# Optimization experiments

Measured on AMD Instinct MI355X. Metric: run time of the kernel, lower is better.

The kernel has to match this reference:

```python
import jax, jax.numpy as jnp
import numpy as np

B, S, D_IN, RANK, D_OUT = 8, 1024, 1280, 64, 1280
DOWN_SIZE = RANK * D_IN      # 81920
UP_SIZE = D_OUT * RANK       # 81920


def setup_inputs() -> dict:
    key = jax.random.key(0)
    k1, k2 = jax.random.split(key)
    x = jax.random.normal(k1, (B, S, D_IN), dtype=jnp.float32)
    # per-image embedding that encodes the dynamic LoRA weights
    embed = jax.random.normal(k2, (B, DOWN_SIZE + UP_SIZE), dtype=jnp.float32) * 0.02
    return {"x": x, "embed": embed}


def reference(x, embed):
    # down_forward: per-sample weight = embed[:, :down_size].view(down_shape)=[rank, d_in]
    # original does x_chunk @ W.T per sample; batched as a single grouped GEMM
    w_down = embed[:, :DOWN_SIZE].reshape(B, RANK, D_IN)   # [B, r, d_in]
    h = jnp.einsum('bsd,brd->bsr', x, w_down)              # x @ W_down.T, batched
    # up_forward: per-sample weight = embed[:, -up_size:].view(up_shape)=[d_out, rank]
    w_up = embed[:, -UP_SIZE:].reshape(B, D_OUT, RANK)     # [B, d_out, r]
    out = jnp.einsum('bsr,bor->bso', h, w_up)              # h @ W_up.T, batched
    return out
```

## Files before the change

### kernel.cpp

```cpp
#include <hip/hip_runtime.h>

#define NB   8
#define S_   1024
#define DIN  1280
#define RANK 64
#define DOUT 1280
#define DOWN (RANK * DIN)
#define EMB  (DOWN + DOUT * RANK)
#define XSTRIDE 1288

typedef __bf16 bf16x8 __attribute__((ext_vector_type(8)));
typedef __bf16 bf16x4 __attribute__((ext_vector_type(4)));
typedef float  f32x4  __attribute__((ext_vector_type(4)));

__device__ __forceinline__ bf16x8 cvt8(float4 f0, float4 f1) {
    bf16x8 v;
    v[0]=(__bf16)f0.x; v[1]=(__bf16)f0.y; v[2]=(__bf16)f0.z; v[3]=(__bf16)f0.w;
    v[4]=(__bf16)f1.x; v[5]=(__bf16)f1.y; v[6]=(__bf16)f1.z; v[7]=(__bf16)f1.w;
    return v;
}

__global__ __launch_bounds__(512, 2) void lora_fused(const float* __restrict__ x,
                                                     const float* __restrict__ embed,
                                                     float* __restrict__ out) {
    __shared__ __bf16 xls[16 * XSTRIDE];
    __shared__ float  pbuf[4][16][20];
    __shared__ __bf16 hld[16][80];

    const int b    = blockIdx.x & 7;
    const int s0   = (blockIdx.x >> 3) * 16;
    const int t    = threadIdx.x;
    const int w    = t >> 6;
    const int l    = t & 63;
    const int quad = l >> 4;
    const int lc   = l & 15;
    const int dq   = quad * 8;

    {
        const int row = t >> 5;
        const int c   = t & 31;
        const float4* src = reinterpret_cast<const float4*>(x + (size_t)(b * S_ + s0 + row) * DIN);
        __bf16* drow = xls + row * XSTRIDE;
#pragma unroll
        for (int j = 0; j < 10; ++j) {
            float4 f = src[c + 32 * j];
            bf16x4 v;
            v[0]=(__bf16)f.x; v[1]=(__bf16)f.y; v[2]=(__bf16)f.z; v[3]=(__bf16)f.w;
            *reinterpret_cast<bf16x4*>(drow + c * 4 + 128 * j) = v;
        }
    }
    __syncthreads();

    const int nt = w & 3;
    const int kh = w >> 2;
    const float*  wdrow  = embed + (size_t)b * EMB + (size_t)(nt * 16 + lc) * DIN + kh * 640;
    const __bf16* xlsrow = xls + lc * XSTRIDE + kh * 640;

    f32x4 acc = {0,0,0,0};
#pragma unroll 5
    for (int ks = 0; ks < 20; ++ks) {
        const int k = ks * 32 + dq;
        bf16x8 af = *reinterpret_cast<const bf16x8*>(xlsrow + k);
        const float4* wp = reinterpret_cast<const float4*>(wdrow + k);
        bf16x8 bf = cvt8(wp[0], wp[1]);
        acc = __builtin_amdgcn_mfma_f32_16x16x32_bf16(af, bf, acc, 0, 0, 0);
    }

    if (kh == 1) {
#pragma unroll
        for (int i = 0; i < 4; ++i) pbuf[nt][quad * 4 + i][lc] = acc[i];
    }
    __syncthreads();
    if (kh == 0) {
#pragma unroll
        for (int i = 0; i < 4; ++i) {
            float v = acc[i] + pbuf[nt][quad * 4 + i][lc];
            hld[quad * 4 + i][nt * 16 + lc] = (__bf16)v;
        }
    }
    __syncthreads();

    bf16x8 ha0 = *reinterpret_cast<const bf16x8*>(&hld[lc][dq]);
    bf16x8 ha1 = *reinterpret_cast<const bf16x8*>(&hld[lc][32 + dq]);
    const float* wu    = embed + (size_t)b * EMB + DOWN;
    float*       obase = out + (size_t)(b * S_ + s0 + quad * 4) * DOUT;

#pragma unroll 2
    for (int tt = 0; tt < 10; ++tt) {
        const int n = w + 8 * tt;
        const int o = n * 16 + lc;
        const float4* wr = reinterpret_cast<const float4*>(wu + (size_t)o * RANK);
        const int q2 = quad * 2;
        bf16x8 b0 = cvt8(wr[q2],     wr[q2 + 1]);
        bf16x8 b1 = cvt8(wr[8 + q2], wr[9 + q2]);
        f32x4 c = {0,0,0,0};
        c = __builtin_amdgcn_mfma_f32_16x16x32_bf16(ha0, b0, c, 0, 0, 0);
        c = __builtin_amdgcn_mfma_f32_16x16x32_bf16(ha1, b1, c, 0, 0, 0);
#pragma unroll
        for (int i = 0; i < 4; ++i)
            obase[(size_t)i * DOUT + o] = c[i];
    }
}

extern "C" void kernel_launch(void* const* d_in, const int* in_sizes, int n_in,
                              void* d_out, int out_size, void* d_ws, size_t ws_size,
                              hipStream_t stream) {
    const float* x     = (const float*)d_in[0];
    const float* embed = (const float*)d_in[1];
    float*       out   = (float*)d_out;
    (void)in_sizes; (void)n_in; (void)out_size; (void)d_ws; (void)ws_size;

    lora_fused<<<dim3(512), dim3(512), 0, stream>>>(x, embed, out);
}
```

Baseline: 124.5 us.

## Software-pipeline embed weight loads with register double buffering in both GEMM stages

The down-projection weight loads from embed are now issued before the x staging and shared-memory barrier, and prefetched one group ahead into double-buffered registers. The up-projection weights for the next output tile are prefetched while the current MFMAs and stores run. The aim is to hide global-load latency behind the x conversion, the barriers and the MFMA work. In exchange, register use rises considerably (roughly 20 float4 buffers plus 10 for x), which may cut occupancy under launch_bounds(512,2) or cause spills.

```diff
diff --git a/kernel.cpp b/kernel.cpp
--- a/kernel.cpp
+++ b/kernel.cpp
@@ -35,70 +35,96 @@
     const int quad = l >> 4;
     const int lc   = l & 15;
     const int dq   = quad * 8;
+    const int q2   = quad * 2;
+
+    const int nt = w & 3;
+    const int kh = w >> 2;
+    const float4* wq =
+        reinterpret_cast<const float4*>(embed + (size_t)b * EMB + (size_t)(nt * 16 + lc) * DIN + kh * 640);
 
     {
         const int row = t >> 5;
         const int c   = t & 31;
         const float4* src = reinterpret_cast<const float4*>(x + (size_t)(b * S_ + s0 + row) * DIN);
+        float4 f[10];
+#pragma unroll
+        for (int j = 0; j < 10; ++j) f[j] = src[c + 32 * j];
+
+        float4 wA[10], wB[10];
+#pragma unroll
+        for (int j = 0; j < 5; ++j) { wA[2*j] = wq[j*8 + q2]; wA[2*j+1] = wq[j*8 + q2 + 1]; }
+
         __bf16* drow = xls + row * XSTRIDE;
 #pragma unroll
         for (int j = 0; j < 10; ++j) {
-            float4 f = src[c + 32 * j];
             bf16x4 v;
-            v[0]=(__bf16)f.x; v[1]=(__bf16)f.y; v[2]=(__bf16)f.z; v[3]=(__bf16)f.w;
+            v[0]=(__bf16)f[j].x; v[1]=(__bf16)f[j].y; v[2]=(__bf16)f[j].z; v[3]=(__bf16)f[j].w;
             *reinterpret_cast<bf16x4*>(drow + c * 4 + 128 * j) = v;
         }
-    }
-    __syncthreads();
+        __syncthreads();
 
-    const int nt = w & 3;
-    const int kh = w >> 2;
-    const float*  wdrow  = embed + (size_t)b * EMB + (size_t)(nt * 16 + lc) * DIN + kh * 640;
-    const __bf16* xlsrow = xls + lc * XSTRIDE + kh * 640;
+        const __bf16* xlsrow = xls + lc * XSTRIDE + kh * 640;
+        f32x4 acc = {0,0,0,0};
+#pragma unroll
+        for (int g = 0; g < 4; ++g) {
+            float4* cur = (g & 1) ? wB : wA;
+            float4* nxt = (g & 1) ? wA : wB;
+            if (g < 3) {
+#pragma unroll
+                for (int j = 0; j < 5; ++j) {
+                    nxt[2*j]   = wq[(g+1)*40 + j*8 + q2];
+                    nxt[2*j+1] = wq[(g+1)*40 + j*8 + q2 + 1];
+                }
+            }
+#pragma unroll
+            for (int j = 0; j < 5; ++j) {
+                const int ks = g * 5 + j;
+                bf16x8 af = *reinterpret_cast<const bf16x8*>(xlsrow + ks * 32 + dq);
+                acc = __builtin_amdgcn_mfma_f32_16x16x32_bf16(af, cvt8(cur[2*j], cur[2*j+1]), acc, 0, 0, 0);
+            }
+        }
 
-    f32x4 acc = {0,0,0,0};
-#pragma unroll 5
-    for (int ks = 0; ks < 20; ++ks) {
-        const int k = ks * 32 + dq;
-        bf16x8 af = *reinterpret_cast<const bf16x8*>(xlsrow + k);
-        const float4* wp = reinterpret_cast<const float4*>(wdrow + k);
-        bf16x8 bf = cvt8(wp[0], wp[1]);
-        acc = __builtin_amdgcn_mfma_f32_16x16x32_bf16(af, bf, acc, 0, 0, 0);
-    }
+        const float* wu = embed + (size_t)b * EMB + DOWN;
+        const float4* wr0 = reinterpret_cast<const float4*>(wu + (size_t)(w * 16 + lc) * RANK);
+        float4 u0 = wr0[q2], u1 = wr0[q2 + 1], u2 = wr0[8 + q2], u3 = wr0[9 + q2];
 
-    if (kh == 1) {
+        if (kh == 1) {
 #pragma unroll
-        for (int i = 0; i < 4; ++i) pbuf[nt][quad * 4 + i][lc] = acc[i];
-    }
-    __syncthreads();
-    if (kh == 0) {
+            for (int i = 0; i < 4; ++i) pbuf[nt][quad * 4 + i][lc] = acc[i];
+        }
+        __syncthreads();
+        if (kh == 0) {
 #pragma unroll
-        for (int i = 0; i < 4; ++i) {
-            float v = acc[i] + pbuf[nt][quad * 4 + i][lc];
-            hld[quad * 4 + i][nt * 16 + lc] = (__bf16)v;
+            for (int i = 0; i < 4; ++i) {
+                float v = acc[i] + pbuf[nt][quad * 4 + i][lc];
+                hld[quad * 4 + i][nt * 16 + lc] = (__bf16)v;
+            }
         }
-    }
-    __syncthreads();
+        __syncthreads();
 
-    bf16x8 ha0 = *reinterpret_cast<const bf16x8*>(&hld[lc][dq]);
-    bf16x8 ha1 = *reinterpret_cast<const bf16x8*>(&hld[lc][32 + dq]);
-    const float* wu    = embed + (size_t)b * EMB + DOWN;
-    float*       obase = out + (size_t)(b * S_ + s0 + quad * 4) * DOUT;
+        bf16x8 ha0 = *reinterpret_cast<const bf16x8*>(&hld[lc][dq]);
+        bf16x8 ha1 = *reinterpret_cast<const bf16x8*>(&hld[lc][32 + dq]);
+        float* obase = out + (size_t)(b * S_ + s0 + quad * 4) * DOUT;
 
-#pragma unroll 2
-    for (int tt = 0; tt < 10; ++tt) {
-        const int n = w + 8 * tt;
-        const int o = n * 16 + lc;
-        const float4* wr = reinterpret_cast<const float4*>(wu + (size_t)o * RANK);
-        const int q2 = quad * 2;
-        bf16x8 b0 = cvt8(wr[q2],     wr[q2 + 1]);
-        bf16x8 b1 = cvt8(wr[8 + q2], wr[9 + q2]);
-        f32x4 c = {0,0,0,0};
-        c = __builtin_amdgcn_mfma_f32_16x16x32_bf16(ha0, b0, c, 0, 0, 0);
-        c = __builtin_amdgcn_mfma_f32_16x16x32_bf16(ha1, b1, c, 0, 0, 0);
 #pragma unroll
-        for (int i = 0; i < 4; ++i)
-            obase[(size_t)i * DOUT + o] = c[i];
+        for (int tt = 0; tt < 10; ++tt) {
+            float4 n0, n1, n2, n3;
+            if (tt < 9) {
+                const float4* wrn =
+                    reinterpret_cast<const float4*>(wu + (size_t)((w + 8 * (tt + 1)) * 16 + lc) * RANK);
+                n0 = wrn[q2]; n1 = wrn[q2 + 1]; n2 = wrn[8 + q2]; n3 = wrn[9 + q2];
+            }
+            bf16x8 b0 = cvt8(u0, u1);
+            bf16x8 b1 = cvt8(u2, u3);
+            f32x4 c = {0,0,0,0};
+            c = __builtin_amdgcn_mfma_f32_16x16x32_bf16(ha0, b0, c, 0, 0, 0);
+            c = __builtin_amdgcn_mfma_f32_16x16x32_bf16(ha1, b1, c, 0, 0, 0);
+            const int o = (w + 8 * tt) * 16 + lc;
+#pragma unroll
+            for (int i = 0; i < 4; ++i)
+                obase[(size_t)i * DOUT + o] = c[i];
+            u0 = n0; u1 = n1; u2 = n2; u3 = n3;
+        }
     }
 }
 
```

Result: no change. 124.0 us (-0.3%).
